# Kernel optimization log

Hardware: AMD Instinct MI355X
Metric: run time of the kernel (lower is better)

## Reference

```python
import jax, jax.numpy as jnp
import numpy as np

# ---- config (matches init_kwargs) ----
B, IN_CH, H, W_SP = 8, 1, 256, 256
WIDTH, M1, M2, NL, OUT_CH = 64, 12, 12, 4, 1
FC_HID = 128


def _gelu(a):
    # torch nn.GELU default = exact erf form
    return jax.nn.gelu(a, approximate=False)


def _spectral_conv2d(x, w1, w2):
    """x: [B, Cin, H, W]; w1/w2: [Cin, Cout, M1, M2, 2] -> [B, Cout, H, W]."""
    Bn, Cin, Hn, Wn = x.shape
    Cout = w1.shape[1]
    x_ft = jnp.fft.rfft2(x, axes=(-2, -1))          # [B, Cin, H, W//2+1] complex
    w1c = w1[..., 0] + 1j * w1[..., 1]
    w2c = w2[..., 0] + 1j * w2[..., 1]
    top = jnp.einsum('bixy,ioxy->boxy', x_ft[:, :, :M1, :M2], w1c)
    bot = jnp.einsum('bixy,ioxy->boxy', x_ft[:, :, -M1:, :M2], w2c)
    out_ft = jnp.zeros((Bn, Cout, Hn, Wn // 2 + 1), dtype=x_ft.dtype)
    out_ft = out_ft.at[:, :, :M1, :M2].set(top)
    out_ft = out_ft.at[:, :, -M1:, :M2].set(bot)
    return jnp.fft.irfft2(out_ft, s=(Hn, Wn), axes=(-2, -1))


def setup_inputs() -> dict:
    key = jax.random.key(0)
    ks = jax.random.split(key, 8)
    scale = 1.0 / (WIDTH * WIDTH)
    inp = {
        'x': jax.random.normal(ks[0], (B, IN_CH, H, W_SP)),
        'fc0_w': jax.random.normal(ks[1], (WIDTH, IN_CH + 2)) * 0.3,
        'fc0_b': jnp.zeros((WIDTH,)),
        # spectral weights stacked over layers: [NL, Cin, Cout, M1, M2, 2]
        'w1': scale * jax.random.uniform(ks[2], (NL, WIDTH, WIDTH, M1, M2, 2)),
        'w2': scale * jax.random.uniform(ks[3], (NL, WIDTH, WIDTH, M1, M2, 2)),
        # 1x1 conv weights: [NL, Cout, Cin] and bias [NL, Cout]
        'pw_w': jax.random.normal(ks[4], (NL, WIDTH, WIDTH)) * (1.0 / np.sqrt(WIDTH)),
        'pw_b': jnp.zeros((NL, WIDTH)),
        'fc1_w': jax.random.normal(ks[5], (FC_HID, WIDTH)) * (1.0 / np.sqrt(WIDTH)),
        'fc1_b': jnp.zeros((FC_HID,)),
        'fc2_w': jax.random.normal(ks[6], (OUT_CH, FC_HID)) * (1.0 / np.sqrt(FC_HID)),
        'fc2_b': jnp.zeros((OUT_CH,)),
    }
    return {k: v.astype(jnp.float32) for k, v in inp.items()}


def reference(x, fc0_w, fc0_b, w1, w2, pw_w, pw_b, fc1_w, fc1_b, fc2_w, fc2_b):
    Bn, _, Hn, Wn = x.shape
    # positional grid in [0, 1], concatenated on channel dim
    gx = jnp.broadcast_to(jnp.linspace(0.0, 1.0, Hn)[None, None, :, None], (Bn, 1, Hn, Wn))
    gy = jnp.broadcast_to(jnp.linspace(0.0, 1.0, Wn)[None, None, None, :], (Bn, 1, Hn, Wn))
    h = jnp.concatenate([x, gx.astype(x.dtype), gy.astype(x.dtype)], axis=1)  # [B, in+2, H, W]
    # lift (fc0): Linear over channels (torch weight layout [out, in])
    h = jnp.einsum('bcxy,wc->bwxy', h, fc0_w) + fc0_b[None, :, None, None]
    for i in range(NL):
        x1 = _spectral_conv2d(h, w1[i], w2[i])
        x2 = jnp.einsum('bixy,oi->boxy', h, pw_w[i]) + pw_b[i][None, :, None, None]
        h = x1 + x2
        if i < NL - 1:
            h = _gelu(h)
    # projection head
    h = jnp.einsum('bwxy,fw->bfxy', h, fc1_w) + fc1_b[None, :, None, None]
    h = _gelu(h)
    h = jnp.einsum('bfxy,of->boxy', h, fc2_w) + fc2_b[None, :, None, None]
    return h  # [B, out_channels, H, W]
```

## Files before the change

### kernel.cpp

```cpp
#include <hip/hip_runtime.h>
#include <hip/hip_bf16.h>

#define FC0_F   0
#define FC0B_F  192
#define PWB_F   16640
#define FC1B_F  25088
#define FC2_F   25216
#define FC2B_F  25344
#define PHW_F   25408
#define PHH_F   31552
#define FLAG_F  44032
#define PWA_HI_U 512
#define PWA_LO_U 16896
#define FC1A_HI_U 33792
#define FC1A_LO_U 41984
#define TWI_HI_U 88192
#define TWI_LO_U 96384
#define TWF_HI_U 104576
#define TWF_LO_U 112768
#define HB_OFF_U  131072
#define GG_OFF_U  33685504
#define FO_OFF_F  18415616
#define WS_NEED   74842112
#define NT11 60161

typedef short bf16x8 __attribute__((ext_vector_type(8)));
typedef float f32x4  __attribute__((ext_vector_type(4)));

union FU10 { float f; unsigned u; };
__device__ __forceinline__ float bfu2f(unsigned short u) { FU10 v; v.u = ((unsigned)u) << 16; return v.f; }
__device__ __forceinline__ unsigned short f2bfu(float f) {
  FU10 v; v.f = f; unsigned b = v.u;
  return (unsigned short)((b + 0x7FFFu + ((b >> 16) & 1u)) >> 16);
}
__device__ __forceinline__ float hunp10(const unsigned* hp, int i) {
  unsigned u = hp[i >> 1];
  return bfu2f((unsigned short)((i & 1) ? (u >> 16) : (u & 0xFFFFu)));
}
__device__ __forceinline__ unsigned pk2bf(float a, float b) {
  return (unsigned)f2bfu(a) | ((unsigned)f2bfu(b) << 16);
}
__device__ __forceinline__ float gelu10(float v) {
  return 0.5f * v * (1.0f + erff(v * 0.7071067811865475f));
}
__device__ __forceinline__ float rdw10(const __hip_bfloat16* h, const float* f,
                                       long i, int isf32) {
  return isf32 ? f[i] : __bfloat162float(h[i]);
}

__global__ __launch_bounds__(256) void kf10_fill(__hip_bfloat16* outH, float code) {
  outH[(size_t)blockIdx.x * 256 + threadIdx.x] = __float2bfloat16(code);
}

__global__ __launch_bounds__(64) void kd10_detect(const unsigned short* Xh, float* Wf) {
  if (threadIdx.x == 0 && blockIdx.x == 0) {
    int ok = 1;
    for (int k = 0; k < 128; ++k) {
      unsigned short u = Xh[2 * k];
      unsigned e = (u >> 7) & 0xFF;
      if (!(u == 0 || (e >= 0x60 && e <= 0x88))) ok = 0;
    }
    Wf[FLAG_F] = ok ? 0.0f : 1.0f;
  }
}

__global__ __launch_bounds__(256) void kt10_tables(
    const __hip_bfloat16* f0h, const float* f0f,
    const __hip_bfloat16* f0bh, const float* f0bf,
    const __hip_bfloat16* pwh, const float* pwf,
    const __hip_bfloat16* pwbh, const float* pwbf,
    const __hip_bfloat16* f1h, const float* f1f,
    const __hip_bfloat16* f1bh, const float* f1bf,
    const __hip_bfloat16* f2h, const float* f2f,
    const __hip_bfloat16* f2bh, const float* f2bf,
    float* Wf) {
  unsigned short* Wu = (unsigned short*)Wf;
  const int isf32 = (Wf[FLAG_F] != 0.0f);
  const int stride = gridDim.x * blockDim.x;
  for (int n0 = blockIdx.x * blockDim.x + threadIdx.x; n0 < NT11; n0 += stride) {
    int n = n0;
    if (n < 192) { Wf[FC0_F + n] = rdw10(f0h, f0f, n, isf32); continue; }
    n -= 192;
    if (n < 64)  { Wf[FC0B_F + n] = rdw10(f0bh, f0bf, n, isf32); continue; }
    n -= 64;
    if (n < 256) { Wf[PWB_F + n] = rdw10(pwbh, pwbf, n, isf32); continue; }
    n -= 256;
    if (n < 8192) {
      float v = rdw10(f1h, f1f, n, isf32);
      unsigned short hi = f2bfu(v);
      Wu[FC1A_HI_U + n] = hi;
      Wu[FC1A_LO_U + n] = f2bfu(v - bfu2f(hi));
      continue;
    }
    n -= 8192;
    if (n < 128) { Wf[FC1B_F + n] = rdw10(f1bh, f1bf, n, isf32); continue; }
    n -= 128;
    if (n < 128) { Wf[FC2_F + n] = rdw10(f2h, f2f, n, isf32); continue; }
    n -= 128;
    if (n < 1)   { Wf[FC2B_F + n] = rdw10(f2bh, f2bf, 0, isf32); continue; }
    n -= 1;
    if (n < 6144) { int w = n / 24, r = n % 24, ky = r >> 1, part = r & 1;
      int idx = (w * ky) & 255; float a = idx * (1.0f/128.0f);
      Wf[PHW_F + n] = part ? sinpif(a) : cospif(a); continue; }
    n -= 6144;
    if (n < 12288) { int xx = n / 48, r = n % 48, kx = r >> 1, part = r & 1;
      int kxa = (kx < 12) ? kx : kx + 232;
      int idx = (xx * kxa) & 255; float a = idx * (1.0f/128.0f);
      Wf[PHH_F + n] = part ? sinpif(a) : cospif(a); continue; }
    n -= 12288;
    if (n < 16384) {
      float v = rdw10(pwh, pwf, n, isf32);
      unsigned short hi = f2bfu(v);
      Wu[PWA_HI_U + n] = hi;
      Wu[PWA_LO_U + n] = f2bfu(v - bfu2f(hi));
      continue;
    }
    n -= 16384;
    if (n < 8192) {
      int w = n >> 5, k = n & 31;
      float v;
      if (k == 0)      v = 1.0f / 65536.0f;
      else if (k < 12) { int idx = (w*k) & 255;
        v =  2.0f * cospif(idx * (1.0f/128.0f)) * (1.0f/65536.0f); }
      else if (k < 23) { int ky = k - 11; int idx = (w*ky) & 255;
        v = -2.0f * sinpif(idx * (1.0f/128.0f)) * (1.0f/65536.0f); }
      else v = 0.0f;
      unsigned short hi = f2bfu(v);
      Wu[TWI_HI_U + n] = hi;
      Wu[TWI_LO_U + n] = f2bfu(v - bfu2f(hi));
      continue;
    }
    n -= 8192;
    {
      int r = n >> 8, w = n & 255;
      float v;
      if (r < 12)      { int idx = (w*r) & 255;  v =  cospif(idx * (1.0f/128.0f)); }
      else if (r < 24) { int ky = r - 12; int idx = (w*ky) & 255;
                         v = -sinpif(idx * (1.0f/128.0f)); }
      else v = 0.0f;
      unsigned short hi = f2bfu(v);
      Wu[TWF_HI_U + n] = hi;
      Wu[TWF_LO_U + n] = f2bfu(v - bfu2f(hi));
    }
  }
}

__device__ void gstep10(const float* Wf, __hip_bfloat16* GG,
                        unsigned* hrow32, float* pbuf, int b, int x) {
  const int t = threadIdx.x;
  const int c = t & 63, q = t >> 6;
  const int cp = c >> 1, hi = c & 1;
  float aR[12], aI[12];
#pragma unroll
  for (int k = 0; k < 12; ++k) { aR[k] = 0.0f; aI[k] = 0.0f; }
  for (int j = 0; j < 64; ++j) {
    int w = q*64 + j;
    unsigned u = hrow32[cp*256 + ((w + 2*cp) & 255)];
    float hv = bfu2f((unsigned short)(hi ? (u >> 16) : (u & 0xFFFFu)));
    const float* ph = Wf + PHW_F + w*24;
#pragma unroll
    for (int k = 0; k < 12; ++k) {
      aR[k] += hv * ph[2*k];
      aI[k] -= hv * ph[2*k + 1];
    }
  }
  __syncthreads();
#pragma unroll
  for (int k = 0; k < 12; ++k) {
    pbuf[q*1600 + c*25 + 2*k]     = aR[k];
    pbuf[q*1600 + c*25 + 2*k + 1] = aI[k];
  }
  __syncthreads();
  unsigned* Grow = (unsigned*)((unsigned short*)GG + (size_t)(b*256 + x)*1536);
#pragma unroll
  for (int j = 0; j < 3; ++j) {
    int p = j*256 + t;
    int cc = p / 12, jj = p % 12;
    int base = cc*25;
    int e0 = (jj < 6) ? (4*jj) : (4*(jj - 6) + 1);
    float s0 = pbuf[base + e0]            + pbuf[1600 + base + e0]
             + pbuf[3200 + base + e0]     + pbuf[4800 + base + e0];
    float s1 = pbuf[base + e0 + 2]        + pbuf[1600 + base + e0 + 2]
             + pbuf[3200 + base + e0 + 2] + pbuf[4800 + base + e0 + 2];
    Grow[p] = pk2bf(s0, s1);
  }
}

__device__ __forceinline__ void row_store10(__hip_bfloat16* HB, const unsigned* hrow32,
                                            int b, int x) {
  uint4* hbW = (uint4*)(HB + (size_t)(b*256 + x)*16384);
  const int t = threadIdx.x;
#pragma unroll
  for (int j = 0; j < 8; ++j) {
    int n = j*256 + t, p = n >> 3, cg = n & 7;
    unsigned vv[4];
#pragma unroll
    for (int m = 0; m < 4; ++m) {
      int cp = cg*4 + m;
      vv[m] = hrow32[cp*256 + ((p + 2*cp) & 255)];
    }
    hbW[n] = make_uint4(vv[0], vv[1], vv[2], vv[3]);
  }
}

__global__ __launch_bounds__(256) void kl10_lift(const __hip_bfloat16* Xh, const float* Xf,
                                                 const float* Wf,
                                                 __hip_bfloat16* HB, __hip_bfloat16* GG) {
  __shared__ __align__(16) char smem[32768];
  unsigned* hrow32 = (unsigned*)smem;
  float* pbuf = (float*)smem;
  const int b = blockIdx.x >> 8, x = blockIdx.x & 255;
  const int w = threadIdx.x;
  const int isf32 = (Wf[FLAG_F] != 0.0f);
  float xv = isf32 ? Xf[(size_t)(b*256 + x)*256 + w]
                   : __bfloat162float(Xh[(size_t)(b*256 + x)*256 + w]);
  float gx = x * (1.0f/255.0f), gy = w * (1.0f/255.0f);
#pragma unroll
  for (int cp = 0; cp < 32; ++cp) {
    int c = cp*2;
    float h0 = xv*Wf[FC0_F + c*3]     + gx*Wf[FC0_F + c*3 + 1]
             + gy*Wf[FC0_F + c*3 + 2] + Wf[FC0B_F + c];
    float h1 = xv*Wf[FC0_F + c*3 + 3] + gx*Wf[FC0_F + c*3 + 4]
             + gy*Wf[FC0_F + c*3 + 5] + Wf[FC0B_F + c + 1];
    hrow32[cp*256 + ((w + 2*cp) & 255)] = pk2bf(h0, h1);
  }
  __syncthreads();
  row_store10(HB, hrow32, b, x);
  gstep10(Wf, GG, hrow32, pbuf, b, x);
}

__global__ __launch_bounds__(256) void ks10_spec(const float* Wf, const __hip_bfloat16* GG,
    const __hip_bfloat16* w1h, const float* w1f,
    const __hip_bfloat16* w2h, const float* w2f,
    float* Fo, int l) {
  __shared__ float pbufA[6400];
  __shared__ float Fbuf[1536];
  const int b = blockIdx.x / 24, kx = blockIdx.x % 24;
  const int t = threadIdx.x;
  const int isf32 = (Wf[FLAG_F] != 0.0f);
  {
    const int i = t & 63, q = t >> 6;
    float fr[12], fi[12];
#pragma unroll
    for (int k = 0; k < 12; ++k) { fr[k] = 0.0f; fi[k] = 0.0f; }
    for (int j = 0; j < 64; ++j) {
      int x = q*64 + j;
      const uint4* gp = (const uint4*)((const unsigned short*)GG
                        + (size_t)(b*256 + x)*1536 + i*24);
      uint4 u0 = gp[0], u1 = gp[1], u2 = gp[2];
      float cc = Wf[PHH_F + x*48 + 2*kx], ss = Wf[PHH_F + x*48 + 2*kx + 1];
      unsigned uu[12] = {u0.x, u0.y, u0.z, u0.w, u1.x, u1.y, u1.z, u1.w,
                         u2.x, u2.y, u2.z, u2.w};
#pragma unroll
      for (int k = 0; k < 12; ++k) {
        unsigned ure = uu[k >> 1], uim = uu[6 + (k >> 1)];
        float gr = bfu2f((unsigned short)((k & 1) ? (ure >> 16) : (ure & 0xFFFFu)));
        float gi = bfu2f((unsigned short)((k & 1) ? (uim >> 16) : (uim & 0xFFFFu)));
        fr[k] += gr*cc + gi*ss;
        fi[k] += gi*cc - gr*ss;
      }
    }
#pragma unroll
    for (int k = 0; k < 12; ++k) {
      pbufA[q*1600 + i*25 + 2*k]     = fr[k];
      pbufA[q*1600 + i*25 + 2*k + 1] = fi[k];
    }
  }
  __syncthreads();
#pragma unroll
  for (int j = 0; j < 6; ++j) {
    int idx = j*256 + t;
    int cc = idx / 24, m = idx - cc*24;
    Fbuf[idx] = pbufA[cc*25 + m] + pbufA[1600 + cc*25 + m]
              + pbufA[3200 + cc*25 + m] + pbufA[4800 + cc*25 + m];
  }
  __syncthreads();
  {
    const int o = t & 63, q = t >> 6;
    float br[12], bi[12];
#pragma unroll
    for (int k = 0; k < 12; ++k) { br[k] = 0.0f; bi[k] = 0.0f; }
    const int kxe = (kx < 12) ? kx : kx - 12;
    const __hip_bfloat16* wh = (kx < 12) ? w1h : w2h;
    const float*         wfp = (kx < 12) ? w1f : w2f;
    for (int i = q*16; i < q*16 + 16; ++i) {
      size_t widx = ((size_t)((l*64 + i)*64 + o))*288 + (size_t)kxe*24;
      float wr_[12], wi_[12];
      if (isf32) {
        const float* wp = wfp + widx;
#pragma unroll
        for (int k = 0; k < 12; ++k) { wr_[k] = wp[2*k]; wi_[k] = wp[2*k + 1]; }
      } else {
        const uint4* wp = (const uint4*)((const unsigned short*)wh + widx);
        uint4 u0 = wp[0], u1 = wp[1], u2 = wp[2];
        unsigned uu[12] = {u0.x, u0.y, u0.z, u0.w, u1.x, u1.y, u1.z, u1.w,
                           u2.x, u2.y, u2.z, u2.w};
#pragma unroll
        for (int k = 0; k < 12; ++k) {
          wr_[k] = bfu2f((unsigned short)(uu[k] & 0xFFFFu));
          wi_[k] = bfu2f((unsigned short)(uu[k] >> 16));
        }
      }
      const float* Fp = Fbuf + i*24;
#pragma unroll
      for (int k = 0; k < 12; ++k) {
        float Fr = Fp[k], Fi = Fp[12 + k];
        br[k] += Fr*wr_[k] - Fi*wi_[k];
        bi[k] += Fr*wi_[k] + Fi*wr_[k];
      }
    }
#pragma unroll
    for (int k = 0; k < 12; ++k) {
      pbufA[q*1536 + k*128 + o*2]     = br[k];
      pbufA[q*1536 + k*128 + o*2 + 1] = bi[k];
    }
  }
  __syncthreads();
#pragma unroll
  for (int j = 0; j < 6; ++j) {
    int n = j*256 + t;
    int ky = n >> 7, r = n & 127;
    Fo[((size_t)(b*12 + ky)*24 + kx)*128 + r] =
        pbufA[n] + pbufA[1536 + n] + pbufA[3072 + n] + pbufA[4608 + n];
  }
}

__global__ __launch_bounds__(256) void kg10_ginv(const float* Wf, const float* Fo,
                                                 __hip_bfloat16* GG) {
  const int blk = blockIdx.x;
  const int b = blk / 96, r = blk % 96, ky = r / 8, xg = r % 8;
  const int t = threadIdx.x;
  const int o = t & 63, xi = t >> 6;
  const float2* Fop = (const float2*)(Fo + (size_t)(b*12 + ky)*24*128) + o;
  float fr[24], fi[24];
#pragma unroll
  for (int kx = 0; kx < 24; ++kx) {
    float2 f = Fop[kx*64];
    fr[kx] = f.x; fi[kx] = f.y;
  }
#pragma unroll
  for (int m = 0; m < 8; ++m) {
    int x = xg*32 + xi + 4*m;
    const float* phx = Wf + PHH_F + x*48;
    float gr = 0.0f, gi = 0.0f;
#pragma unroll
    for (int kx = 0; kx < 24; ++kx) {
      float cc = phx[2*kx], ss = phx[2*kx + 1];
      gr += fr[kx]*cc - fi[kx]*ss;
      gi += fr[kx]*ss + fi[kx]*cc;
    }
    unsigned* GGrow = (unsigned*)((unsigned short*)GG + (size_t)(b*256 + x)*1536);
    GGrow[ky*64 + o] = pk2bf(gr, gi);
  }
}

__global__ __launch_bounds__(256) void ky12_layer(const float* __restrict__ Wf,
                                                  __hip_bfloat16* __restrict__ HB,
                                                  __hip_bfloat16* __restrict__ GG,
                                                  __hip_bfloat16* __restrict__ outH,
                                                  float* __restrict__ outF,
                                                  int l, int last) {
  __shared__ __align__(16) char smem[36864];
  unsigned short* gbT   = (unsigned short*)(smem + 32768);
  unsigned*       gbT32 = (unsigned*)(smem + 32768);
  const unsigned short* Wu = (const unsigned short*)Wf;
  const int b = blockIdx.x >> 8, x = blockIdx.x & 255;
  const int t = threadIdx.x;
  const int l15 = t & 15, g = (t >> 4) & 3, wv = t >> 6;

  unsigned short* HBu = (unsigned short*)(HB + (size_t)(b*256 + x)*16384);
  unsigned short* GGu = (unsigned short*)GG + (size_t)(b*256 + x)*1536;

  { int o = t >> 2, cu = t & 3; gbT32[o*16 + 12 + cu] = 0u; }
  {
    const unsigned* g2row = (const unsigned*)GGu;
#pragma unroll
    for (int j = 0; j < 3; ++j) {
      int n = j*256 + t; unsigned u = g2row[n];
      int ky = n >> 6, o = n & 63;
      gbT[o*32 + ky] = (unsigned short)(u & 0xFFFFu);
      gbT[o*32 + (ky ? (11 + ky) : 23)] = (unsigned short)(u >> 16);
    }
  }
  const int w0w = wv*64;
  bf16x8 bh[4][2];
#pragma unroll
  for (int nt = 0; nt < 4; ++nt) {
    int wpx = w0w + nt*16 + l15;
#pragma unroll
    for (int kt = 0; kt < 2; ++kt)
      bh[nt][kt] = *(const bf16x8*)(HBu + (size_t)wpx*64 + kt*32 + g*8);
  }
  bf16x8 bi[4][2];
#pragma unroll
  for (int nt = 0; nt < 4; ++nt) {
    int wpx = w0w + nt*16 + l15;
    bi[nt][0] = *(const bf16x8*)(Wu + TWI_HI_U + wpx*32 + g*8);
    bi[nt][1] = *(const bf16x8*)(Wu + TWI_LO_U + wpx*32 + g*8);
  }
  bf16x8 apw[4][2][2];
#pragma unroll
  for (int mt = 0; mt < 4; ++mt)
#pragma unroll
    for (int kt = 0; kt < 2; ++kt) {
      int off = l*4096 + (mt*16 + l15)*64 + kt*32 + g*8;
      apw[mt][kt][0] = *(const bf16x8*)(Wu + PWA_HI_U + off);
      apw[mt][kt][1] = *(const bf16x8*)(Wu + PWA_LO_U + off);
    }
  float bias[4][4];
#pragma unroll
  for (int mt = 0; mt < 4; ++mt)
#pragma unroll
    for (int r = 0; r < 4; ++r)
      bias[mt][r] = Wf[PWB_F + l*64 + mt*16 + g*4 + r];
  __syncthreads();
  bf16x8 ainv[4];
#pragma unroll
  for (int mt = 0; mt < 4; ++mt)
    ainv[mt] = *(const bf16x8*)(gbT + (mt*16 + l15)*32 + g*8);

#pragma unroll
  for (int nt = 0; nt < 4; ++nt) {
    const int wpx = w0w + nt*16 + l15;
#pragma unroll
    for (int mt = 0; mt < 4; ++mt) {
      f32x4 acc = {bias[mt][0], bias[mt][1], bias[mt][2], bias[mt][3]};
      acc = __builtin_amdgcn_mfma_f32_16x16x32_bf16(ainv[mt],      bi[nt][0], acc, 0, 0, 0);
      acc = __builtin_amdgcn_mfma_f32_16x16x32_bf16(ainv[mt],      bi[nt][1], acc, 0, 0, 0);
      acc = __builtin_amdgcn_mfma_f32_16x16x32_bf16(apw[mt][0][0], bh[nt][0], acc, 0, 0, 0);
      acc = __builtin_amdgcn_mfma_f32_16x16x32_bf16(apw[mt][0][1], bh[nt][0], acc, 0, 0, 0);
      acc = __builtin_amdgcn_mfma_f32_16x16x32_bf16(apw[mt][1][0], bh[nt][1], acc, 0, 0, 0);
      acc = __builtin_amdgcn_mfma_f32_16x16x32_bf16(apw[mt][1][1], bh[nt][1], acc, 0, 0, 0);
      float v0 = acc[0], v1 = acc[1], v2 = acc[2], v3 = acc[3];
      if (!last) { v0 = gelu10(v0); v1 = gelu10(v1); v2 = gelu10(v2); v3 = gelu10(v3); }
      const int c0 = mt*16 + g*4;
      uint2 pk; pk.x = pk2bf(v0, v1); pk.y = pk2bf(v2, v3);
      if (!last) {
        *(uint2*)(HBu + (size_t)wpx*64 + c0) = pk;
        *(unsigned short*)(smem + (((c0+0)*512 + wpx*2) ^ (((c0+0) & 7) << 4))) = f2bfu(v0);
        *(unsigned short*)(smem + (((c0+1)*512 + wpx*2) ^ (((c0+1) & 7) << 4))) = f2bfu(v1);
        *(unsigned short*)(smem + (((c0+2)*512 + wpx*2) ^ (((c0+2) & 7) << 4))) = f2bfu(v2);
        *(unsigned short*)(smem + (((c0+3)*512 + wpx*2) ^ (((c0+3) & 7) << 4))) = f2bfu(v3);
      } else {
        *(uint2*)(smem + ((wpx*128 + c0*2) ^ ((wpx & 7) << 4))) = pk;
      }
    }
  }

  if (!last) {
    __syncthreads();
    f32x4 g0 = {0.f, 0.f, 0.f, 0.f}, g1 = {0.f, 0.f, 0.f, 0.f};
    const int crow = wv*16 + l15;
    const int rswz = (crow & 7) << 4;
#pragma unroll
    for (int kk = 0; kk < 8; ++kk) {
      const int k0 = kk*32;
      bf16x8 af  = *(const bf16x8*)(smem + ((crow*512 + (k0 + g*8)*2) ^ rswz));
      bf16x8 b0h = *(const bf16x8*)(Wu + TWF_HI_U + l15*256 + k0 + g*8);
      bf16x8 b0l = *(const bf16x8*)(Wu + TWF_LO_U + l15*256 + k0 + g*8);
      bf16x8 b1h = *(const bf16x8*)(Wu + TWF_HI_U + (16 + l15)*256 + k0 + g*8);
      bf16x8 b1l = *(const bf16x8*)(Wu + TWF_LO_U + (16 + l15)*256 + k0 + g*8);
      g0 = __builtin_amdgcn_mfma_f32_16x16x32_bf16(af, b0h, g0, 0, 0, 0);
      g0 = __builtin_amdgcn_mfma_f32_16x16x32_bf16(af, b0l, g0, 0, 0, 0);
      g1 = __builtin_amdgcn_mfma_f32_16x16x32_bf16(af, b1h, g1, 0, 0, 0);
      g1 = __builtin_amdgcn_mfma_f32_16x16x32_bf16(af, b1l, g1, 0, 0, 0);
    }
#pragma unroll
    for (int ntk = 0; ntk < 2; ++ntk) {
      int kyt = ntk*16 + l15;
      if (kyt < 24) {
        f32x4 gg = ntk ? g1 : g0;
#pragma unroll
        for (int rr = 0; rr < 4; ++rr)
          gbT[(wv*16 + g*4 + rr)*24 + kyt] = f2bfu(gg[rr]);
      }
    }
    __syncthreads();
    unsigned* GGrow = (unsigned*)GGu;
    const unsigned* st32 = (const unsigned*)gbT;
#pragma unroll
    for (int j = 0; j < 3; ++j) GGrow[j*256 + t] = st32[j*256 + t];
  } else {
    __syncthreads();
    const int isf32 = (Wf[FLAG_F] != 0.0f);
    bf16x8 bh2[4][2];
#pragma unroll
    for (int nt = 0; nt < 4; ++nt) {
      int wpx = w0w + nt*16 + l15;
#pragma unroll
      for (int kt = 0; kt < 2; ++kt)
        bh2[nt][kt] = *(const bf16x8*)(smem +
            ((wpx*128 + kt*64 + g*16) ^ ((wpx & 7) << 4)));
    }
    float s[4] = {0.0f, 0.0f, 0.0f, 0.0f};
#pragma unroll 2
    for (int mt = 0; mt < 8; ++mt) {
      const int arow = (mt*16 + l15)*64 + g*8;
      bf16x8 a0h = *(const bf16x8*)(Wu + FC1A_HI_U + arow);
      bf16x8 a0l = *(const bf16x8*)(Wu + FC1A_LO_U + arow);
      bf16x8 a1h = *(const bf16x8*)(Wu + FC1A_HI_U + arow + 32);
      bf16x8 a1l = *(const bf16x8*)(Wu + FC1A_LO_U + arow + 32);
      float f1b[4], f2v[4];
#pragma unroll
      for (int r = 0; r < 4; ++r) {
        f1b[r] = Wf[FC1B_F + mt*16 + g*4 + r];
        f2v[r] = Wf[FC2_F  + mt*16 + g*4 + r];
      }
#pragma unroll
      for (int nt = 0; nt < 4; ++nt) {
        f32x4 acc = {f1b[0], f1b[1], f1b[2], f1b[3]};
        acc = __builtin_amdgcn_mfma_f32_16x16x32_bf16(a0h, bh2[nt][0], acc, 0, 0, 0);
        acc = __builtin_amdgcn_mfma_f32_16x16x32_bf16(a0l, bh2[nt][0], acc, 0, 0, 0);
        acc = __builtin_amdgcn_mfma_f32_16x16x32_bf16(a1h, bh2[nt][1], acc, 0, 0, 0);
        acc = __builtin_amdgcn_mfma_f32_16x16x32_bf16(a1l, bh2[nt][1], acc, 0, 0, 0);
#pragma unroll
        for (int r = 0; r < 4; ++r)
          s[nt] += gelu10(acc[r]) * f2v[r];
      }
    }
    const float fc2b = Wf[FC2B_F];
#pragma unroll
    for (int nt = 0; nt < 4; ++nt) {
      float v = s[nt];
      v += __shfl_xor(v, 16);
      v += __shfl_xor(v, 32);
      if (g == 0) {
        size_t idx = (size_t)(b*256 + x)*256 + (w0w + nt*16 + l15);
        if (isf32) outF[idx] = v + fc2b;
        else       outH[idx] = __float2bfloat16(v + fc2b);
      }
    }
  }
}

extern "C" void kernel_launch(void* const* d_in, const int* in_sizes, int n_in,
                              void* d_out, int out_size, void* d_ws, size_t ws_size,
                              hipStream_t stream) {
  (void)out_size;
  __hip_bfloat16* outH = (__hip_bfloat16*)d_out;
  float*          outF = (float*)d_out;
  float*          Wf   = (float*)d_ws;
  __hip_bfloat16* HB   = (__hip_bfloat16*)d_ws + HB_OFF_U;
  __hip_bfloat16* GG   = (__hip_bfloat16*)d_ws + GG_OFF_U;
  float*          Fo   = (float*)d_ws + FO_OFF_F;

  static const int EXP_SZ[11] = {524288, 192, 64, 4718592, 4718592,
                                 16384, 256, 8192, 128, 128, 1};
  if (n_in != 11) { kf10_fill<<<2048, 256, 0, stream>>>(outH, 27648.0f); return; }
  for (int i = 0; i < 11; ++i) {
    if (in_sizes[i] != EXP_SZ[i]) {
      kf10_fill<<<2048, 256, 0, stream>>>(outH, 28672.0f + 256.0f * (float)i);
      return;
    }
  }
  if (ws_size < (size_t)WS_NEED) {
    int q = (int)(ws_size >> 25); if (q > 31) q = 31;
    kf10_fill<<<2048, 256, 0, stream>>>(outH, 4096.0f + 32.0f * (float)q);
    return;
  }

  kd10_detect<<<1, 64, 0, stream>>>((const unsigned short*)d_in[0], Wf);
  kt10_tables<<<64, 256, 0, stream>>>(
      (const __hip_bfloat16*)d_in[1], (const float*)d_in[1],
      (const __hip_bfloat16*)d_in[2], (const float*)d_in[2],
      (const __hip_bfloat16*)d_in[5], (const float*)d_in[5],
      (const __hip_bfloat16*)d_in[6], (const float*)d_in[6],
      (const __hip_bfloat16*)d_in[7], (const float*)d_in[7],
      (const __hip_bfloat16*)d_in[8], (const float*)d_in[8],
      (const __hip_bfloat16*)d_in[9], (const float*)d_in[9],
      (const __hip_bfloat16*)d_in[10], (const float*)d_in[10],
      Wf);
  kl10_lift<<<2048, 256, 0, stream>>>((const __hip_bfloat16*)d_in[0],
                                      (const float*)d_in[0], Wf, HB, GG);
  for (int l = 0; l < 4; ++l) {
    ks10_spec<<<192, 256, 0, stream>>>(Wf, GG,
        (const __hip_bfloat16*)d_in[3], (const float*)d_in[3],
        (const __hip_bfloat16*)d_in[4], (const float*)d_in[4],
        Fo, l);
    kg10_ginv<<<768, 256, 0, stream>>>(Wf, Fo, GG);
    ky12_layer<<<2048, 256, 0, stream>>>(Wf, HB, GG, outH, outF, l, (l == 3) ? 1 : 0);
  }
}
```

Baseline: 735.3 us.

## Fuse inverse x-DFT into layer kernel and remap block order across batches

Removes the separate kg10_ginv kernel. Each ky13_layer block now computes its own row's inverse x-direction partial DFT directly from Fo, instead of reading a GG row written by a previous launch. This cuts one launch per layer and a global round-trip of the GG intermediate, but every row block now redoes a 24-term complex sum per (ky,o) and reads Fo redundantly. Block indices in lift, spec and layer are also permuted to interleave batches across CUs, and the shared buffer is reused, which needs extra barriers.

```diff
diff --git a/kernel.cpp b/kernel.cpp
--- a/kernel.cpp
+++ b/kernel.cpp
@@ -32,10 +32,6 @@
 __device__ __forceinline__ unsigned short f2bfu(float f) {
   FU10 v; v.f = f; unsigned b = v.u;
   return (unsigned short)((b + 0x7FFFu + ((b >> 16) & 1u)) >> 16);
-}
-__device__ __forceinline__ float hunp10(const unsigned* hp, int i) {
-  unsigned u = hp[i >> 1];
-  return bfu2f((unsigned short)((i & 1) ? (u >> 16) : (u & 0xFFFFu)));
 }
 __device__ __forceinline__ unsigned pk2bf(float a, float b) {
   return (unsigned)f2bfu(a) | ((unsigned)f2bfu(b) << 16);
@@ -209,7 +205,8 @@
   __shared__ __align__(16) char smem[32768];
   unsigned* hrow32 = (unsigned*)smem;
   float* pbuf = (float*)smem;
-  const int b = blockIdx.x >> 8, x = blockIdx.x & 255;
+  const int rid = ((blockIdx.x & 7) << 8) | (blockIdx.x >> 3);
+  const int b = rid >> 8, x = rid & 255;
   const int w = threadIdx.x;
   const int isf32 = (Wf[FLAG_F] != 0.0f);
   float xv = isf32 ? Xf[(size_t)(b*256 + x)*256 + w]
@@ -235,7 +232,8 @@
     float* Fo, int l) {
   __shared__ float pbufA[6400];
   __shared__ float Fbuf[1536];
-  const int b = blockIdx.x / 24, kx = blockIdx.x % 24;
+  const int blk = (blockIdx.x & 7) * 24 + (blockIdx.x >> 3);
+  const int b = blk / 24, kx = blk % 24;
   const int t = threadIdx.x;
   const int isf32 = (Wf[FLAG_F] != 0.0f);
   {
@@ -325,72 +323,55 @@
   }
 }
 
-__global__ __launch_bounds__(256) void kg10_ginv(const float* Wf, const float* Fo,
-                                                 __hip_bfloat16* GG) {
-  const int blk = blockIdx.x;
-  const int b = blk / 96, r = blk % 96, ky = r / 8, xg = r % 8;
-  const int t = threadIdx.x;
-  const int o = t & 63, xi = t >> 6;
-  const float2* Fop = (const float2*)(Fo + (size_t)(b*12 + ky)*24*128) + o;
-  float fr[24], fi[24];
-#pragma unroll
-  for (int kx = 0; kx < 24; ++kx) {
-    float2 f = Fop[kx*64];
-    fr[kx] = f.x; fi[kx] = f.y;
-  }
-#pragma unroll
-  for (int m = 0; m < 8; ++m) {
-    int x = xg*32 + xi + 4*m;
-    const float* phx = Wf + PHH_F + x*48;
-    float gr = 0.0f, gi = 0.0f;
-#pragma unroll
-    for (int kx = 0; kx < 24; ++kx) {
-      float cc = phx[2*kx], ss = phx[2*kx + 1];
-      gr += fr[kx]*cc - fi[kx]*ss;
-      gi += fr[kx]*ss + fi[kx]*cc;
-    }
-    unsigned* GGrow = (unsigned*)((unsigned short*)GG + (size_t)(b*256 + x)*1536);
-    GGrow[ky*64 + o] = pk2bf(gr, gi);
-  }
-}
-
-__global__ __launch_bounds__(256) void ky12_layer(const float* __restrict__ Wf,
+__global__ __launch_bounds__(256) void ky13_layer(const float* __restrict__ Wf,
                                                   __hip_bfloat16* __restrict__ HB,
                                                   __hip_bfloat16* __restrict__ GG,
+                                                  const float* __restrict__ Fo,
                                                   __hip_bfloat16* __restrict__ outH,
                                                   float* __restrict__ outF,
                                                   int l, int last) {
-  __shared__ __align__(16) char smem[36864];
-  unsigned short* gbT   = (unsigned short*)(smem + 32768);
-  unsigned*       gbT32 = (unsigned*)(smem + 32768);
+  __shared__ __align__(16) char smem[32768];
+  unsigned short* gbT   = (unsigned short*)smem;
+  unsigned*       gbT32 = (unsigned*)smem;
   const unsigned short* Wu = (const unsigned short*)Wf;
-  const int b = blockIdx.x >> 8, x = blockIdx.x & 255;
+  const int rid = ((blockIdx.x & 7) << 8) | (blockIdx.x >> 3);
+  const int b = rid >> 8, x = rid & 255;
   const int t = threadIdx.x;
   const int l15 = t & 15, g = (t >> 4) & 3, wv = t >> 6;
 
   unsigned short* HBu = (unsigned short*)(HB + (size_t)(b*256 + x)*16384);
   unsigned short* GGu = (unsigned short*)GG + (size_t)(b*256 + x)*1536;
 
+  const int w0w = wv*64;
+  bf16x8 bh[4][2];
+#pragma unroll
+  for (int nt = 0; nt < 4; ++nt) {
+    int wpx = w0w + nt*16 + l15;
+#pragma unroll
+    for (int kt = 0; kt < 2; ++kt)
+      bh[nt][kt] = *(const bf16x8*)(HBu + (size_t)wpx*64 + kt*32 + g*8);
+  }
+
   { int o = t >> 2, cu = t & 3; gbT32[o*16 + 12 + cu] = 0u; }
   {
-    const unsigned* g2row = (const unsigned*)GGu;
-#pragma unroll
+    const float* phx = Wf + PHH_F + x*48;
+#pragma unroll 1
     for (int j = 0; j < 3; ++j) {
-      int n = j*256 + t; unsigned u = g2row[n];
-      int ky = n >> 6, o = n & 63;
-      gbT[o*32 + ky] = (unsigned short)(u & 0xFFFFu);
-      gbT[o*32 + (ky ? (11 + ky) : 23)] = (unsigned short)(u >> 16);
-    }
-  }
-  const int w0w = wv*64;
-  bf16x8 bh[4][2];
-#pragma unroll
-  for (int nt = 0; nt < 4; ++nt) {
-    int wpx = w0w + nt*16 + l15;
-#pragma unroll
-    for (int kt = 0; kt < 2; ++kt)
-      bh[nt][kt] = *(const bf16x8*)(HBu + (size_t)wpx*64 + kt*32 + g*8);
-  }
+      int p = j*256 + t; int ky = p >> 6, o = p & 63;
+      const float2* Fop = (const float2*)(Fo + (size_t)(b*12 + ky)*3072) + o;
+      float gr = 0.0f, gi = 0.0f;
+#pragma unroll
+      for (int kx = 0; kx < 24; ++kx) {
+        float2 f = Fop[kx*64];
+        float cc = phx[2*kx], ss = phx[2*kx + 1];
+        gr += f.x*cc - f.y*ss;
+        gi += f.x*ss + f.y*cc;
+      }
+      gbT[o*32 + ky] = f2bfu(gr);
+      gbT[o*32 + (ky ? (11 + ky) : 23)] = f2bfu(gi);
+    }
+  }
+
   bf16x8 bi[4][2];
 #pragma unroll
   for (int nt = 0; nt < 4; ++nt) {
@@ -413,11 +394,13 @@
 #pragma unroll
     for (int r = 0; r < 4; ++r)
       bias[mt][r] = Wf[PWB_F + l*64 + mt*16 + g*4 + r];
+
   __syncthreads();
   bf16x8 ainv[4];
 #pragma unroll
   for (int mt = 0; mt < 4; ++mt)
     ainv[mt] = *(const bf16x8*)(gbT + (mt*16 + l15)*32 + g*8);
+  __syncthreads();
 
 #pragma unroll
   for (int nt = 0; nt < 4; ++nt) {
@@ -465,6 +448,7 @@
       g1 = __builtin_amdgcn_mfma_f32_16x16x32_bf16(af, b1h, g1, 0, 0, 0);
       g1 = __builtin_amdgcn_mfma_f32_16x16x32_bf16(af, b1l, g1, 0, 0, 0);
     }
+    __syncthreads();
 #pragma unroll
     for (int ntk = 0; ntk < 2; ++ntk) {
       int kyt = ntk*16 + l15;
@@ -577,7 +561,7 @@
         (const __hip_bfloat16*)d_in[3], (const float*)d_in[3],
         (const __hip_bfloat16*)d_in[4], (const float*)d_in[4],
         Fo, l);
-    kg10_ginv<<<768, 256, 0, stream>>>(Wf, Fo, GG);
-    ky12_layer<<<2048, 256, 0, stream>>>(Wf, HB, GG, outH, outF, l, (l == 3) ? 1 : 0);
-  }
-}
+    ky13_layer<<<2048, 256, 0, stream>>>(Wf, HB, GG, Fo, outH, outF,
+                                         l, (l == 3) ? 1 : 0);
+  }
+}
```

Result: no change. 749.4 us (+1.9%).
